# Kernel tuning notes

Measured on AMD Instinct MI355X. Metric: run time of the kernel, lower is better.

Reference implementation:

```python
import jax, jax.numpy as jnp
import numpy as np


def setup_inputs() -> dict:
    key = jax.random.key(0)
    kq, kk, kv, km = jax.random.split(key, 4)
    B, H, S, D = 4, 16, 2048, 64
    query = jax.random.normal(kq, (B, H, S, D), dtype=jnp.float32)
    k = jax.random.normal(kk, (B, H, S, D), dtype=jnp.float32)
    value = jax.random.normal(kv, (B, H, S, D), dtype=jnp.float32)
    mask = jax.random.randint(km, (B, S, S), 0, 2, dtype=jnp.int32)
    return {"query": query, "key": k, "value": value, "mask": mask}


def reference(query, key, value, mask):
    # query/key/value: [B, H, S, D]; mask: [B, S, S] (0 = masked out)
    d = query.shape[-1]
    scale = 1.0 / jnp.sqrt(jnp.asarray(d, dtype=query.dtype))
    scores = jnp.einsum('bhqd,bhkd->bhqk', query, key) * scale
    m = (mask[:, None, :, :] == 0)  # broadcast over heads, matches mask.unsqueeze(1).eq(0)
    min_value = jnp.finfo(scores.dtype).min
    scores = jnp.where(m, min_value, scores)
    attn = jax.nn.softmax(scores, axis=-1)
    attn = jnp.where(m, jnp.asarray(0.0, attn.dtype), attn)
    out = jnp.einsum('bhqk,bhkd->bhqd', attn, value)
    return (out, attn)
```

## Files before the change

kernel.cpp:

```cpp
#include <hip/hip_runtime.h>
#include <hip/hip_bf16.h>


typedef __attribute__((ext_vector_type(8))) short bf16x8;
typedef __attribute__((ext_vector_type(4))) short bf16x4;
typedef __attribute__((ext_vector_type(4))) float f32x4;
typedef __attribute__((ext_vector_type(4))) int i32x4;

#define MFMA32(A, B, C) __builtin_amdgcn_mfma_f32_16x16x32_bf16((A), (B), (C), 0, 0, 0)

constexpr int Bsz = 4, Hsz = 16, Ssz = 2048, Dsz = 64;
constexpr int KBLK = 64;
constexpr int NT   = Ssz / KBLK;
constexpr float SCALE = 0.125f;

static __device__ __forceinline__ short f2bf(float f) {
  __hip_bfloat16 h = __float2bfloat16(f);
  return __builtin_bit_cast(short, h);
}

static __device__ __forceinline__ void wg_barrier() {
  __builtin_amdgcn_sched_barrier(0);
  asm volatile("s_waitcnt lgkmcnt(0)" ::: "memory");
  __builtin_amdgcn_sched_barrier(0);
  __builtin_amdgcn_s_barrier();
  __builtin_amdgcn_sched_barrier(0);
}

__global__ __launch_bounds__(512, 8)
void attn_denom(const float* __restrict__ Qg, const float* __restrict__ Kg,
                const int* __restrict__ Mg, float* __restrict__ wsL,
                unsigned short* __restrict__ wsM)
{
  __shared__ short sK[2][KBLK][72];

  const int qt = blockIdx.x, bh = blockIdx.y;
  const int q0 = qt * 128;
  const int tid = threadIdx.x, lane = tid & 63, w = tid >> 6;
  const int lr = lane & 15, lg = lane >> 4;

  const size_t bhSD = (size_t)bh * (Ssz * Dsz);
  const float* Qb = Qg + bhSD;
  const float* Kb = Kg + bhSD;
  const int b = bh >> 4;
  const int qrow = q0 + w * 16 + lr;
  const int* Mrow = Mg + ((size_t)b * Ssz + qrow) * Ssz;
  unsigned short* wsMq = wsM + (size_t)(b * Ssz + qrow) * (NT * 4) + lg;

  bf16x8 qf[2];
  {
    const float* qp = Qb + (size_t)qrow * Dsz + lg * 8;
#pragma unroll
    for (int h = 0; h < 2; ++h) {
      f32x4 a = *(const f32x4*)(qp + h * 32);
      f32x4 c2 = *(const f32x4*)(qp + h * 32 + 4);
      bf16x8 t;
#pragma unroll
      for (int j = 0; j < 4; ++j) { t[j] = f2bf(a[j] * SCALE); t[4 + j] = f2bf(c2[j] * SCALE); }
      qf[h] = t;
    }
  }

  const int krow = tid >> 3, kd0 = (tid & 7) * 8;
  {
    const float* kp = Kb + (size_t)krow * Dsz + kd0;
    f32x4 a = *(const f32x4*)kp, c2 = *(const f32x4*)(kp + 4);
    bf16x8 t;
#pragma unroll
    for (int j = 0; j < 4; ++j) { t[j] = f2bf(a[j]); t[4 + j] = f2bf(c2[j]); }
    *(bf16x8*)(&sK[0][krow][kd0]) = t;
  }
  wg_barrier();

  float lacc = 0.f;
  for (int t = 0; t < NT; ++t) {
    const int cur = t & 1;
    f32x4 ka = {0.f,0.f,0.f,0.f}, kb2 = {0.f,0.f,0.f,0.f};
    if (t + 1 < NT) {
      const float* kp = Kb + (size_t)((t + 1) * KBLK + krow) * Dsz + kd0;
      ka  = *(const f32x4*)kp;
      kb2 = *(const f32x4*)(kp + 4);
    }
    unsigned bits = 0;
#pragma unroll
    for (int cb = 0; cb < 4; ++cb) {
      const short* kr = &sK[cur][cb * 16 + lr][0];
      bf16x8 a0 = *(const bf16x8*)(kr + lg * 8);
      bf16x8 a1 = *(const bf16x8*)(kr + 32 + lg * 8);
      f32x4 c = {0.f, 0.f, 0.f, 0.f};
      c = MFMA32(a0, qf[0], c);
      c = MFMA32(a1, qf[1], c);
      i32x4 mv = *(const i32x4*)(Mrow + t * KBLK + cb * 16 + lg * 4);
#pragma unroll
      for (int r = 0; r < 4; ++r) {
        lacc += mv[r] ? __expf(c[r]) : 0.f;
        bits |= (mv[r] ? 1u : 0u) << (cb * 4 + r);
      }
    }
    wsMq[t * 4] = (unsigned short)bits;
    if (t + 1 < NT) {
      bf16x8 t2;
#pragma unroll
      for (int j = 0; j < 4; ++j) { t2[j] = f2bf(ka[j]); t2[4 + j] = f2bf(kb2[j]); }
      *(bf16x8*)(&sK[cur ^ 1][krow][kd0]) = t2;
    }
    wg_barrier();
  }

  lacc += __shfl_xor(lacc, 16, 64);
  lacc += __shfl_xor(lacc, 32, 64);
  if (lane < 16)
    wsL[(size_t)bh * Ssz + qrow] = (lacc > 0.f) ? 1.f / lacc : 0.f;
}

__global__ __launch_bounds__(512, 8)
void attn_emit(const float* __restrict__ Qg, const float* __restrict__ Kg,
               const float* __restrict__ Vg, const float* __restrict__ wsL,
               const unsigned short* __restrict__ wsM,
               float* __restrict__ Og, float* __restrict__ Ag)
{
  __shared__ __align__(16) char smem[49152];
  auto sK  = (short(*)[KBLK][72])(smem);
  auto sVt = (short(*)[Dsz][72])(smem + 2 * 9216);
  auto sO  = (float(*)[68])(smem);

  const int qt = blockIdx.x, bh = blockIdx.y;
  const int q0 = qt * 64;
  const int tid = threadIdx.x, lane = tid & 63, wid = tid >> 6;
  const int wq = wid >> 1, wk = wid & 1;
  const int lr = lane & 15, lg = lane >> 4;

  const size_t bhSD = (size_t)bh * (Ssz * Dsz);
  const float* Qb = Qg + bhSD;
  const float* Kb = Kg + bhSD;
  const float* Vb = Vg + bhSD;
  const int b = bh >> 4;
  float* Ob = Og + bhSD;
  float* Ab = Ag + (size_t)bh * ((size_t)Ssz * Ssz);

  const int qrow = q0 + wq * 16 + lr;
  float* Arow = Ab + (size_t)qrow * Ssz;
  const float invl = wsL[(size_t)bh * Ssz + qrow];
  const unsigned short* wsMq = wsM + (size_t)(b * Ssz + qrow) * (NT * 4) + lg;
  const int mshift = wk * 8;

  bf16x8 qf[2];
  {
    const float* qp = Qb + (size_t)qrow * Dsz + lg * 8;
#pragma unroll
    for (int h = 0; h < 2; ++h) {
      f32x4 a = *(const f32x4*)(qp + h * 32);
      f32x4 c2 = *(const f32x4*)(qp + h * 32 + 4);
      bf16x8 t;
#pragma unroll
      for (int j = 0; j < 4; ++j) { t[j] = f2bf(a[j] * SCALE); t[4 + j] = f2bf(c2[j] * SCALE); }
      qf[h] = t;
    }
  }

  const int krow = tid >> 3;
  const int kd0  = (tid & 7) * 8;
  const int vkv  = tid & 63;
  const int vd0  = (tid >> 6) * 8;
  const int kb0  = wk * 32 + lg * 4;

  f32x4 oacc[4] = {{0,0,0,0},{0,0,0,0},{0,0,0,0},{0,0,0,0}};

  {
    const float* kp = Kb + (size_t)krow * Dsz + kd0;
    f32x4 a = *(const f32x4*)kp, c2 = *(const f32x4*)(kp + 4);
    bf16x8 t;
#pragma unroll
    for (int j = 0; j < 4; ++j) { t[j] = f2bf(a[j]); t[4 + j] = f2bf(c2[j]); }
    *(bf16x8*)(&sK[0][krow][kd0]) = t;

    const float* vp = Vb + (size_t)vkv * Dsz + vd0;
    f32x4 va = *(const f32x4*)vp, vb = *(const f32x4*)(vp + 4);
#pragma unroll
    for (int j = 0; j < 4; ++j) {
      sVt[0][vd0 + j][vkv]     = f2bf(va[j]);
      sVt[0][vd0 + 4 + j][vkv] = f2bf(vb[j]);
    }
  }
  unsigned mbn = wsMq[0];
  wg_barrier();

  for (int t = 0; t < NT; ++t) {
    const int cur = t & 1;
    const unsigned mb = mbn;
    f32x4 ka = {0.f,0.f,0.f,0.f}, kb2 = {0.f,0.f,0.f,0.f};
    f32x4 va = {0.f,0.f,0.f,0.f}, vb2 = {0.f,0.f,0.f,0.f};
    if (t + 1 < NT) {
      const float* kp = Kb + (size_t)((t + 1) * KBLK + krow) * Dsz + kd0;
      ka  = *(const f32x4*)kp;
      kb2 = *(const f32x4*)(kp + 4);
      const float* vp = Vb + (size_t)((t + 1) * KBLK + vkv) * Dsz + vd0;
      va  = *(const f32x4*)vp;
      vb2 = *(const f32x4*)(vp + 4);
      mbn  = wsMq[(t + 1) * 4];
    }
    __builtin_amdgcn_s_setprio(1);
    const short* kr0 = &sK[cur][wk * 32 + lr][0];
    const short* kr1 = &sK[cur][wk * 32 + 16 + lr][0];
    bf16x8 a00 = *(const bf16x8*)(kr0 + lg * 8);
    bf16x8 a01 = *(const bf16x8*)(kr0 + 32 + lg * 8);
    bf16x8 a10 = *(const bf16x8*)(kr1 + lg * 8);
    bf16x8 a11 = *(const bf16x8*)(kr1 + 32 + lg * 8);
    f32x4 c0 = {0.f,0.f,0.f,0.f}, c1 = {0.f,0.f,0.f,0.f};
    c0 = MFMA32(a00, qf[0], c0);
    c0 = MFMA32(a01, qf[1], c0);
    c1 = MFMA32(a10, qf[0], c1);
    c1 = MFMA32(a11, qf[1], c1);
    f32x4 p0, p1;
#pragma unroll
    for (int r = 0; r < 4; ++r) {
      p0[r] = ((mb >> (mshift + r))     & 1u) ? __expf(c0[r]) * invl : 0.f;
      p1[r] = ((mb >> (mshift + 4 + r)) & 1u) ? __expf(c1[r]) * invl : 0.f;
    }
    __builtin_nontemporal_store(p0, (f32x4*)(Arow + t * KBLK + kb0));
    __builtin_nontemporal_store(p1, (f32x4*)(Arow + t * KBLK + kb0 + 16));
    bf16x4 pf0 = {f2bf(p0[0]), f2bf(p0[1]), f2bf(p0[2]), f2bf(p0[3])};
    bf16x4 pf1 = {f2bf(p1[0]), f2bf(p1[1]), f2bf(p1[2]), f2bf(p1[3])};
    {
      bf16x4 vf0 = *(const bf16x4*)(&sVt[cur][0 * 16 + lr][wk * 32 + lg * 4]);
      bf16x4 vf1 = *(const bf16x4*)(&sVt[cur][1 * 16 + lr][wk * 32 + lg * 4]);
      bf16x4 vf2 = *(const bf16x4*)(&sVt[cur][2 * 16 + lr][wk * 32 + lg * 4]);
      bf16x4 vf3 = *(const bf16x4*)(&sVt[cur][3 * 16 + lr][wk * 32 + lg * 4]);
      asm volatile(
        "s_nop 1\n\t"
        "v_mfma_f32_16x16x16_bf16 %0, %4, %5, %0\n\t"
        "v_mfma_f32_16x16x16_bf16 %1, %4, %6, %1\n\t"
        "v_mfma_f32_16x16x16_bf16 %2, %4, %7, %2\n\t"
        "v_mfma_f32_16x16x16_bf16 %3, %4, %8, %3\n\t"
        "s_nop 2"
        : "+v"(oacc[0]), "+v"(oacc[1]), "+v"(oacc[2]), "+v"(oacc[3])
        : "v"(pf0), "v"(vf0), "v"(vf1), "v"(vf2), "v"(vf3));
    }
    {
      bf16x4 vf0 = *(const bf16x4*)(&sVt[cur][0 * 16 + lr][wk * 32 + 16 + lg * 4]);
      bf16x4 vf1 = *(const bf16x4*)(&sVt[cur][1 * 16 + lr][wk * 32 + 16 + lg * 4]);
      bf16x4 vf2 = *(const bf16x4*)(&sVt[cur][2 * 16 + lr][wk * 32 + 16 + lg * 4]);
      bf16x4 vf3 = *(const bf16x4*)(&sVt[cur][3 * 16 + lr][wk * 32 + 16 + lg * 4]);
      asm volatile(
        "s_nop 1\n\t"
        "v_mfma_f32_16x16x16_bf16 %0, %4, %5, %0\n\t"
        "v_mfma_f32_16x16x16_bf16 %1, %4, %6, %1\n\t"
        "v_mfma_f32_16x16x16_bf16 %2, %4, %7, %2\n\t"
        "v_mfma_f32_16x16x16_bf16 %3, %4, %8, %3\n\t"
        "s_nop 2"
        : "+v"(oacc[0]), "+v"(oacc[1]), "+v"(oacc[2]), "+v"(oacc[3])
        : "v"(pf1), "v"(vf0), "v"(vf1), "v"(vf2), "v"(vf3));
    }
    __builtin_amdgcn_s_setprio(0);
    if (t + 1 < NT) {
      bf16x8 t2;
#pragma unroll
      for (int j = 0; j < 4; ++j) { t2[j] = f2bf(ka[j]); t2[4 + j] = f2bf(kb2[j]); }
      *(bf16x8*)(&sK[cur ^ 1][krow][kd0]) = t2;
#pragma unroll
      for (int j = 0; j < 4; ++j) {
        sVt[cur ^ 1][vd0 + j][vkv]     = f2bf(va[j]);
        sVt[cur ^ 1][vd0 + 4 + j][vkv] = f2bf(vb2[j]);
      }
    }
    wg_barrier();
  }

  asm volatile("s_nop 7\n\ts_nop 7" :::);

  if (wk == 0) {
#pragma unroll
    for (int nb = 0; nb < 4; ++nb)
#pragma unroll
      for (int r = 0; r < 4; ++r)
        sO[wq * 16 + lg * 4 + r][nb * 16 + lr] = oacc[nb][r];
  }
  wg_barrier();
  if (wk == 1) {
#pragma unroll
    for (int nb = 0; nb < 4; ++nb)
#pragma unroll
      for (int r = 0; r < 4; ++r) {
        float v = sO[wq * 16 + lg * 4 + r][nb * 16 + lr] + oacc[nb][r];
        __builtin_nontemporal_store(v, Ob + (size_t)(q0 + wq * 16 + lg * 4 + r) * Dsz + nb * 16 + lr);
      }
  }
}

extern "C" void kernel_launch(void* const* d_in, const int* in_sizes, int n_in,
                              void* d_out, int out_size, void* d_ws, size_t ws_size,
                              hipStream_t stream) {
  const float* Q = (const float*)d_in[0];
  const float* K = (const float*)d_in[1];
  const float* V = (const float*)d_in[2];
  const int*   M = (const int*)d_in[3];
  float* Out  = (float*)d_out;
  float* Attn = Out + (size_t)Bsz * Hsz * Ssz * Dsz;
  float* wsL = (float*)d_ws;
  unsigned short* wsM = (unsigned short*)((char*)d_ws + (size_t)Bsz * Hsz * Ssz * sizeof(float));
  attn_denom<<<dim3(Ssz / 128, Bsz * Hsz), 512, 0, stream>>>(Q, K, M, wsL, wsM);
  attn_emit <<<dim3(Ssz / 64,  Bsz * Hsz), 512, 0, stream>>>(Q, K, V, wsL, wsM, Out, Attn);
}
```

Measured before the change: 464.2 us.

## Deepen K/V prefetch to two tiles, swizzle block order, relax launch bounds

The emit loop is unrolled by two so global loads for tile t+2 are issued while tile t computes, with two register sets holding in-flight K/V data. This gives each load more time to land before its LDS write. Both kernels now use a 1D grid with an XCD-aware swizzle, so blocks sharing the same (b,h) K/V land on the same chiplet's L2. The emit kernel's minimum-occupancy hint drops from 8 to 6 to make room for the extra registers, which may lower occupancy.

```diff
diff --git a/kernel.cpp b/kernel.cpp
--- a/kernel.cpp
+++ b/kernel.cpp
@@ -34,7 +34,10 @@
 {
   __shared__ short sK[2][KBLK][72];
 
-  const int qt = blockIdx.x, bh = blockIdx.y;
+  const int bid = blockIdx.x;
+  const int lin = ((bid & 7) << 7) | (bid >> 3);
+  const int bh  = lin >> 4;
+  const int qt  = lin & 15;
   const int q0 = qt * 128;
   const int tid = threadIdx.x, lane = tid & 63, w = tid >> 6;
   const int lr = lane & 15, lg = lane >> 4;
@@ -113,7 +116,7 @@
     wsL[(size_t)bh * Ssz + qrow] = (lacc > 0.f) ? 1.f / lacc : 0.f;
 }
 
-__global__ __launch_bounds__(512, 8)
+__global__ __launch_bounds__(512, 6)
 void attn_emit(const float* __restrict__ Qg, const float* __restrict__ Kg,
                const float* __restrict__ Vg, const float* __restrict__ wsL,
                const unsigned short* __restrict__ wsM,
@@ -124,7 +127,10 @@
   auto sVt = (short(*)[Dsz][72])(smem + 2 * 9216);
   auto sO  = (float(*)[68])(smem);
 
-  const int qt = blockIdx.x, bh = blockIdx.y;
+  const int bid = blockIdx.x;
+  const int lin = ((bid & 7) << 8) | (bid >> 3);
+  const int bh  = lin >> 5;
+  const int qt  = lin & 31;
   const int q0 = qt * 64;
   const int tid = threadIdx.x, lane = tid & 63, wid = tid >> 6;
   const int wq = wid >> 1, wk = wid & 1;
@@ -166,42 +172,30 @@
 
   f32x4 oacc[4] = {{0,0,0,0},{0,0,0,0},{0,0,0,0},{0,0,0,0}};
 
-  {
-    const float* kp = Kb + (size_t)krow * Dsz + kd0;
-    f32x4 a = *(const f32x4*)kp, c2 = *(const f32x4*)(kp + 4);
-    bf16x8 t;
-#pragma unroll
-    for (int j = 0; j < 4; ++j) { t[j] = f2bf(a[j]); t[4 + j] = f2bf(c2[j]); }
-    *(bf16x8*)(&sK[0][krow][kd0]) = t;
-
-    const float* vp = Vb + (size_t)vkv * Dsz + vd0;
-    f32x4 va = *(const f32x4*)vp, vb = *(const f32x4*)(vp + 4);
+  auto g_load = [&](int t, f32x4& ka, f32x4& kb2, f32x4& va, f32x4& vb2) {
+    const float* kp = Kb + (size_t)(t * KBLK + krow) * Dsz + kd0;
+    ka  = *(const f32x4*)kp;
+    kb2 = *(const f32x4*)(kp + 4);
+    const float* vp = Vb + (size_t)(t * KBLK + vkv) * Dsz + vd0;
+    va  = *(const f32x4*)vp;
+    vb2 = *(const f32x4*)(vp + 4);
+  };
+  auto lds_write = [&](int buf, const f32x4& ka, const f32x4& kb2,
+                       const f32x4& va, const f32x4& vb2) {
+    bf16x8 t2;
+#pragma unroll
+    for (int j = 0; j < 4; ++j) { t2[j] = f2bf(ka[j]); t2[4 + j] = f2bf(kb2[j]); }
+    *(bf16x8*)(&sK[buf][krow][kd0]) = t2;
 #pragma unroll
     for (int j = 0; j < 4; ++j) {
-      sVt[0][vd0 + j][vkv]     = f2bf(va[j]);
-      sVt[0][vd0 + 4 + j][vkv] = f2bf(vb[j]);
-    }
-  }
-  unsigned mbn = wsMq[0];
-  wg_barrier();
-
-  for (int t = 0; t < NT; ++t) {
-    const int cur = t & 1;
-    const unsigned mb = mbn;
-    f32x4 ka = {0.f,0.f,0.f,0.f}, kb2 = {0.f,0.f,0.f,0.f};
-    f32x4 va = {0.f,0.f,0.f,0.f}, vb2 = {0.f,0.f,0.f,0.f};
-    if (t + 1 < NT) {
-      const float* kp = Kb + (size_t)((t + 1) * KBLK + krow) * Dsz + kd0;
-      ka  = *(const f32x4*)kp;
-      kb2 = *(const f32x4*)(kp + 4);
-      const float* vp = Vb + (size_t)((t + 1) * KBLK + vkv) * Dsz + vd0;
-      va  = *(const f32x4*)vp;
-      vb2 = *(const f32x4*)(vp + 4);
-      mbn  = wsMq[(t + 1) * 4];
-    }
+      sVt[buf][vd0 + j][vkv]     = f2bf(va[j]);
+      sVt[buf][vd0 + 4 + j][vkv] = f2bf(vb2[j]);
+    }
+  };
+  auto compute_tile = [&](int buf, int t, unsigned mb) {
     __builtin_amdgcn_s_setprio(1);
-    const short* kr0 = &sK[cur][wk * 32 + lr][0];
-    const short* kr1 = &sK[cur][wk * 32 + 16 + lr][0];
+    const short* kr0 = &sK[buf][wk * 32 + lr][0];
+    const short* kr1 = &sK[buf][wk * 32 + 16 + lr][0];
     bf16x8 a00 = *(const bf16x8*)(kr0 + lg * 8);
     bf16x8 a01 = *(const bf16x8*)(kr0 + 32 + lg * 8);
     bf16x8 a10 = *(const bf16x8*)(kr1 + lg * 8);
@@ -222,10 +216,10 @@
     bf16x4 pf0 = {f2bf(p0[0]), f2bf(p0[1]), f2bf(p0[2]), f2bf(p0[3])};
     bf16x4 pf1 = {f2bf(p1[0]), f2bf(p1[1]), f2bf(p1[2]), f2bf(p1[3])};
     {
-      bf16x4 vf0 = *(const bf16x4*)(&sVt[cur][0 * 16 + lr][wk * 32 + lg * 4]);
-      bf16x4 vf1 = *(const bf16x4*)(&sVt[cur][1 * 16 + lr][wk * 32 + lg * 4]);
-      bf16x4 vf2 = *(const bf16x4*)(&sVt[cur][2 * 16 + lr][wk * 32 + lg * 4]);
-      bf16x4 vf3 = *(const bf16x4*)(&sVt[cur][3 * 16 + lr][wk * 32 + lg * 4]);
+      bf16x4 vf0 = *(const bf16x4*)(&sVt[buf][0 * 16 + lr][wk * 32 + lg * 4]);
+      bf16x4 vf1 = *(const bf16x4*)(&sVt[buf][1 * 16 + lr][wk * 32 + lg * 4]);
+      bf16x4 vf2 = *(const bf16x4*)(&sVt[buf][2 * 16 + lr][wk * 32 + lg * 4]);
+      bf16x4 vf3 = *(const bf16x4*)(&sVt[buf][3 * 16 + lr][wk * 32 + lg * 4]);
       asm volatile(
         "s_nop 1\n\t"
         "v_mfma_f32_16x16x16_bf16 %0, %4, %5, %0\n\t"
@@ -237,10 +231,10 @@
         : "v"(pf0), "v"(vf0), "v"(vf1), "v"(vf2), "v"(vf3));
     }
     {
-      bf16x4 vf0 = *(const bf16x4*)(&sVt[cur][0 * 16 + lr][wk * 32 + 16 + lg * 4]);
-      bf16x4 vf1 = *(const bf16x4*)(&sVt[cur][1 * 16 + lr][wk * 32 + 16 + lg * 4]);
-      bf16x4 vf2 = *(const bf16x4*)(&sVt[cur][2 * 16 + lr][wk * 32 + 16 + lg * 4]);
-      bf16x4 vf3 = *(const bf16x4*)(&sVt[cur][3 * 16 + lr][wk * 32 + 16 + lg * 4]);
+      bf16x4 vf0 = *(const bf16x4*)(&sVt[buf][0 * 16 + lr][wk * 32 + 16 + lg * 4]);
+      bf16x4 vf1 = *(const bf16x4*)(&sVt[buf][1 * 16 + lr][wk * 32 + 16 + lg * 4]);
+      bf16x4 vf2 = *(const bf16x4*)(&sVt[buf][2 * 16 + lr][wk * 32 + 16 + lg * 4]);
+      bf16x4 vf3 = *(const bf16x4*)(&sVt[buf][3 * 16 + lr][wk * 32 + 16 + lg * 4]);
       asm volatile(
         "s_nop 1\n\t"
         "v_mfma_f32_16x16x16_bf16 %0, %4, %5, %0\n\t"
@@ -252,17 +246,29 @@
         : "v"(pf1), "v"(vf0), "v"(vf1), "v"(vf2), "v"(vf3));
     }
     __builtin_amdgcn_s_setprio(0);
-    if (t + 1 < NT) {
-      bf16x8 t2;
-#pragma unroll
-      for (int j = 0; j < 4; ++j) { t2[j] = f2bf(ka[j]); t2[4 + j] = f2bf(kb2[j]); }
-      *(bf16x8*)(&sK[cur ^ 1][krow][kd0]) = t2;
-#pragma unroll
-      for (int j = 0; j < 4; ++j) {
-        sVt[cur ^ 1][vd0 + j][vkv]     = f2bf(va[j]);
-        sVt[cur ^ 1][vd0 + 4 + j][vkv] = f2bf(vb2[j]);
-      }
-    }
+  };
+
+  f32x4 kaA, kbA, vaA, vbA, kaB, kbB, vaB, vbB;
+  {
+    f32x4 k0a, k0b, v0a, v0b;
+    g_load(0, k0a, k0b, v0a, v0b);
+    lds_write(0, k0a, k0b, v0a, v0b);
+  }
+  g_load(1, kaA, kbA, vaA, vbA);
+  unsigned mb0 = wsMq[0];
+  unsigned mb1 = wsMq[4];
+  wg_barrier();
+
+  for (int t = 0; t < NT; t += 2) {
+    if (t + 2 < NT) g_load(t + 2, kaB, kbB, vaB, vbB);
+    compute_tile(0, t, mb0);
+    if (t + 2 < NT) mb0 = wsMq[(t + 2) * 4];
+    lds_write(1, kaA, kbA, vaA, vbA);
+    wg_barrier();
+    if (t + 3 < NT) g_load(t + 3, kaA, kbA, vaA, vbA);
+    compute_tile(1, t + 1, mb1);
+    if (t + 3 < NT) mb1 = wsMq[(t + 3) * 4];
+    if (t + 2 < NT) lds_write(0, kaB, kbB, vaB, vbB);
     wg_barrier();
   }
 
@@ -298,6 +304,6 @@
   float* Attn = Out + (size_t)Bsz * Hsz * Ssz * Dsz;
   float* wsL = (float*)d_ws;
   unsigned short* wsM = (unsigned short*)((char*)d_ws + (size_t)Bsz * Hsz * Ssz * sizeof(float));
-  attn_denom<<<dim3(Ssz / 128, Bsz * Hsz), 512, 0, stream>>>(Q, K, M, wsL, wsM);
-  attn_emit <<<dim3(Ssz / 64,  Bsz * Hsz), 512, 0, stream>>>(Q, K, V, wsL, wsM, Out, Attn);
-}
+  attn_denom<<<dim3(1024), 512, 0, stream>>>(Q, K, M, wsL, wsM);
+  attn_emit <<<dim3(2048), 512, 0, stream>>>(Q, K, V, wsL, wsM, Out, Attn);
+}
```

Result: slower. 873.1 us (+88.1%).
